# Kernel tuning notes

Hardware: AMD Instinct MI355X
Metric: run time of the kernel (lower is better)

## Reference

```python
import jax, jax.numpy as jnp
import numpy as np

L, B, D = 2048, 2, 1024
H, DK, DV = 16, 64, 64
SPAN = 128
LN_EPS = 1e-5


def setup_inputs() -> dict:
    key = jax.random.key(0)
    ks = jax.random.split(key, 8)
    s_qk = np.sqrt(2.0 / (D + DK)).astype(np.float32)
    s_v = np.sqrt(2.0 / (D + DV)).astype(np.float32)
    return {
        "query": jax.random.normal(ks[0], (L, B, D), jnp.float32),
        "key": jax.random.normal(ks[1], (L, B, D), jnp.float32),
        "value": jax.random.normal(ks[2], (L, B, D), jnp.float32),
        "Wq": jax.random.normal(ks[3], (D, H * DK), jnp.float32) * s_qk,
        "bq": jnp.zeros((H * DK,), jnp.float32),
        "Wk": jax.random.normal(ks[4], (D, H * DK), jnp.float32) * s_qk,
        "bk": jnp.zeros((H * DK,), jnp.float32),
        "Wv": jax.random.normal(ks[5], (D, H * DV), jnp.float32) * s_v,
        "bv": jnp.zeros((H * DV,), jnp.float32),
        "Wfc": jax.random.normal(ks[6], (H * DV, D), jnp.float32) * np.sqrt(2.0 / (H * DV + D)).astype(np.float32),
        "bfc": jnp.zeros((D,), jnp.float32),
        "gamma": jnp.ones((D,), jnp.float32),
        "beta": jnp.zeros((D,), jnp.float32),
    }


def reference(query, key, value, Wq, bq, Wk, bk, Wv, bv, Wfc, bfc, gamma, beta):
    l, b, d = query.shape
    # projections: (l,b,H*dk) -> (H,b,l,dk)   [torch rearrange 'l b (head k) -> head b l k']
    q = (query @ Wq + bq).reshape(l, b, H, DK).transpose(2, 1, 0, 3)
    k = (key @ Wk + bk).reshape(l, b, H, DK).transpose(2, 1, 0, 3)
    v = (value @ Wv + bv).reshape(l, b, H, DV).transpose(2, 1, 0, 3)
    scores = jnp.einsum("hblk,hbtk->hblt", q, k) / jnp.sqrt(jnp.float32(DK))
    # banded additive mask: keep |j - i| <= SPAN
    idx = jnp.arange(l)
    band = jnp.abs(idx[None, :] - idx[:, None]) <= SPAN  # (l, l)
    scores = jnp.where(band[None, None], scores, -jnp.inf)
    attn = jax.nn.softmax(scores, axis=-1)
    out = jnp.einsum("hblt,hbtv->hblv", attn, v)
    # 'head b l v -> l b (head v)'
    out = out.transpose(2, 1, 0, 3).reshape(l, b, H * DV)
    out = out @ Wfc + bfc  # dropout p=0.0 -> identity
    y = out + query  # residual
    mu = jnp.mean(y, axis=-1, keepdims=True)
    var = jnp.mean(jnp.square(y - mu), axis=-1, keepdims=True)
    y = (y - mu) * jax.lax.rsqrt(var + LN_EPS) * gamma + beta
    return (y, attn)
```

## Files before the change

kernel.cpp:

```cpp
#include <hip/hip_runtime.h>
#include <stdint.h>

#define L_SEQ 2048
#define BB 2
#define DD 1024
#define NH 16
#define SPAN 128

typedef __attribute__((ext_vector_type(8))) short short8;
typedef __attribute__((ext_vector_type(4))) float floatx4;

__device__ __forceinline__ short f32_bf16(float f) {
  uint32_t u = __float_as_uint(f);
  u += 0x7FFFu + ((u >> 16) & 1u);
  return (short)(u >> 16);
}

__global__ __launch_bounds__(256) void k_convert(
    const float* __restrict__ s0, const float* __restrict__ s1, const float* __restrict__ s2,
    short* __restrict__ d0, short* __restrict__ d1, short* __restrict__ d2) {
  const float* s = blockIdx.y == 0 ? s0 : (blockIdx.y == 1 ? s1 : s2);
  short* d = blockIdx.y == 0 ? d0 : (blockIdx.y == 1 ? d1 : d2);
  int i = blockIdx.x * 256 + threadIdx.x;
  float4 v = ((const float4*)s)[i];
  short4 o;
  o.x = f32_bf16(v.x); o.y = f32_bf16(v.y); o.z = f32_bf16(v.z); o.w = f32_bf16(v.w);
  ((short4*)d)[i] = o;
}

__global__ __launch_bounds__(256) void k_transpose(
    const float* __restrict__ w0, const float* __restrict__ w1,
    const float* __restrict__ w2, const float* __restrict__ w3,
    short* __restrict__ dst) {
  __shared__ float tile[32][33];
  const float* src = blockIdx.z == 0 ? w0 : blockIdx.z == 1 ? w1 : blockIdx.z == 2 ? w2 : w3;
  short* out = dst + (size_t)blockIdx.z * (DD * DD);
  int bx = blockIdx.x * 32, by = blockIdx.y * 32;
  int tx = threadIdx.x, ty = threadIdx.y;
#pragma unroll
  for (int r = 0; r < 32; r += 8)
    tile[ty + r][tx] = src[(size_t)(by + ty + r) * DD + bx + tx];
  __syncthreads();
#pragma unroll
  for (int r = 0; r < 32; r += 8)
    out[(size_t)(bx + ty + r) * DD + by + tx] = f32_bf16(tile[tx][ty + r]);
}

__global__ __launch_bounds__(256) void k_zero(float4* __restrict__ p) {
  size_t i = (size_t)blockIdx.x * 256 + threadIdx.x;
  float4 z = {0.f, 0.f, 0.f, 0.f};
#pragma unroll
  for (int w = 0; w < 8; ++w) p[i + (size_t)w * 4194304] = z;
}

#define BM 128
#define BN 128
#define BK 32
#define LDK 56

__device__ __forceinline__ void gemm_core(const short* __restrict__ A,
                                          const short* __restrict__ BT,
                                          floatx4 acc[4][4], int bm0, int bn0) {
  __shared__ short As[BM * LDK];
  __shared__ short Bs[BN * LDK];
  int tid = threadIdx.x;
  int wave = tid >> 6, lane = tid & 63;
  int li = lane & 15, quad = lane >> 4;
  int wm = (wave & 1) * 64, wn = (wave >> 1) * 64;
  int srow = tid >> 1, scol = (tid & 1) * 16;
  const short* gA = A + (size_t)(bm0 + srow) * DD + scol;
  const short* gB = BT + (size_t)(bn0 + srow) * DD + scol;
  short* sA = &As[srow * LDK + scol];
  short* sB = &Bs[srow * LDK + scol];
  for (int k0 = 0; k0 < DD; k0 += BK) {
    short8 a0 = *(const short8*)(gA + k0);
    short8 a1 = *(const short8*)(gA + k0 + 8);
    short8 b0 = *(const short8*)(gB + k0);
    short8 b1 = *(const short8*)(gB + k0 + 8);
    __syncthreads();
    *(short8*)sA = a0;
    *(short8*)(sA + 8) = a1;
    *(short8*)sB = b0;
    *(short8*)(sB + 8) = b1;
    __syncthreads();
    short8 af[4], bf[4];
#pragma unroll
    for (int t = 0; t < 4; ++t) {
      af[t] = *(const short8*)&As[(wm + t * 16 + li) * LDK + quad * 8];
      bf[t] = *(const short8*)&Bs[(wn + t * 16 + li) * LDK + quad * 8];
    }
#pragma unroll
    for (int tm = 0; tm < 4; ++tm)
#pragma unroll
      for (int tn = 0; tn < 4; ++tn)
        acc[tm][tn] = __builtin_amdgcn_mfma_f32_16x16x32_bf16(af[tm], bf[tn], acc[tm][tn], 0, 0, 0);
  }
}

__global__ __launch_bounds__(256) void k_proj(
    const short* __restrict__ xq, const short* __restrict__ xk, const short* __restrict__ xv,
    const short* __restrict__ WT,
    const float* __restrict__ bq, const float* __restrict__ bk, const float* __restrict__ bv,
    short* __restrict__ qo, short* __restrict__ ko, short* __restrict__ vTo) {
  int mode = blockIdx.z;
  const short* A = mode == 0 ? xq : (mode == 1 ? xk : xv);
  const short* BT = WT + (size_t)mode * DD * DD;
  const float* bias = mode == 0 ? bq : (mode == 1 ? bk : bv);
  floatx4 acc[4][4] = {};
  int bm0 = blockIdx.y * BM, bn0 = blockIdx.x * BN;
  gemm_core(A, BT, acc, bm0, bn0);

  int tid = threadIdx.x;
  int wave = tid >> 6, lane = tid & 63;
  int li = lane & 15, quad = lane >> 4;
  int wm = (wave & 1) * 64, wn = (wave >> 1) * 64;
  short* dst01 = (mode == 0) ? qo : ko;
#pragma unroll
  for (int tm = 0; tm < 4; ++tm) {
#pragma unroll
    for (int tn = 0; tn < 4; ++tn) {
      int gn = bn0 + wn + tn * 16 + li;
      float bs = bias[gn];
      int h = gn >> 6, dk = gn & 63;
#pragma unroll
      for (int r = 0; r < 4; ++r) {
        int gm = bm0 + wm + tm * 16 + quad * 4 + r;
        int l = gm >> 1, b = gm & 1;
        short bvv = f32_bf16(acc[tm][tn][r] + bs);
        if (mode < 2)
          dst01[(((size_t)h * BB + b) * L_SEQ + l) * 64 + dk] = bvv;
        else
          vTo[(((size_t)h * BB + b) * 64 + dk) * L_SEQ + l] = bvv;
      }
    }
  }
}

__global__ __launch_bounds__(64) void k_attn(
    const short* __restrict__ qw, const short* __restrict__ kw, const short* __restrict__ vTw,
    float* __restrict__ attn_out, short* __restrict__ ctx) {
  __shared__ short P[16 * 296];
  const int i0 = blockIdx.x * 16;
  const int hb = blockIdx.y;
  const int lane = threadIdx.x;
  const int li = lane & 15, quad = lane >> 4;
  const short* Q = qw + (size_t)hb * L_SEQ * 64;
  const short* K = kw + (size_t)hb * L_SEQ * 64;
  const short* VT = vTw + (size_t)hb * 64 * L_SEQ;
  float* Aout = attn_out + (size_t)hb * L_SEQ * L_SEQ;

  short8 qf0 = *(const short8*)(Q + (size_t)(i0 + li) * 64 + quad * 8);
  short8 qf1 = *(const short8*)(Q + (size_t)(i0 + li) * 64 + 32 + quad * 8);

  floatx4 S[17];
  const int jbase = i0 - SPAN;
#pragma unroll
  for (int t = 0; t < 17; ++t) {
    int j0 = jbase + t * 16;
    floatx4 acc = {0.f, 0.f, 0.f, 0.f};
    if (j0 >= 0 && j0 < L_SEQ) {
      const short* kp = K + (size_t)(j0 + li) * 64 + quad * 8;
      short8 kf0 = *(const short8*)kp;
      short8 kf1 = *(const short8*)(kp + 32);
      acc = __builtin_amdgcn_mfma_f32_16x16x32_bf16(qf0, kf0, acc, 0, 0, 0);
      acc = __builtin_amdgcn_mfma_f32_16x16x32_bf16(qf1, kf1, acc, 0, 0, 0);
    }
    S[t] = acc;
  }
  float mrow[4] = {-1e30f, -1e30f, -1e30f, -1e30f};
#pragma unroll
  for (int t = 0; t < 17; ++t) {
    int j0 = jbase + t * 16;
    bool tvalid = (j0 >= 0) && (j0 < L_SEQ);
    int j = j0 + li;
#pragma unroll
    for (int r = 0; r < 4; ++r) {
      int i = i0 + quad * 4 + r;
      bool inband = tvalid && (j >= i - SPAN) && (j <= i + SPAN);
      float s = inband ? S[t][r] * 0.125f : -1e30f;
      S[t][r] = s;
      mrow[r] = fmaxf(mrow[r], s);
    }
  }
#pragma unroll
  for (int m = 1; m <= 8; m <<= 1)
#pragma unroll
    for (int r = 0; r < 4; ++r) mrow[r] = fmaxf(mrow[r], __shfl_xor(mrow[r], m));
  float lsum[4] = {0.f, 0.f, 0.f, 0.f};
#pragma unroll
  for (int t = 0; t < 17; ++t)
#pragma unroll
    for (int r = 0; r < 4; ++r) {
      float p = __expf(S[t][r] - mrow[r]);
      S[t][r] = p;
      lsum[r] += p;
    }
#pragma unroll
  for (int m = 1; m <= 8; m <<= 1)
#pragma unroll
    for (int r = 0; r < 4; ++r) lsum[r] += __shfl_xor(lsum[r], m);
  float inv[4];
#pragma unroll
  for (int r = 0; r < 4; ++r) inv[r] = 1.0f / lsum[r];

#pragma unroll
  for (int c = 0; c < 4; ++c) P[li * 296 + 272 + quad * 4 + c] = 0;
#pragma unroll
  for (int t = 0; t < 17; ++t) {
    int j0 = jbase + t * 16;
    bool tvalid = (j0 >= 0) && (j0 < L_SEQ);
#pragma unroll
    for (int r = 0; r < 4; ++r) {
      int irow = quad * 4 + r;
      float p = S[t][r] * inv[r];
      P[irow * 296 + t * 16 + li] = f32_bf16(p);
      if (tvalid) Aout[(size_t)(i0 + irow) * L_SEQ + j0 + li] = p;
    }
  }
  __syncthreads();
  floatx4 O[4] = {};
#pragma unroll
  for (int c = 0; c < 9; ++c) {
    short8 pf = *(const short8*)&P[li * 296 + c * 32 + quad * 8];
    int jg = jbase + c * 32 + quad * 8;
    int jc = (jg >= 0 && jg < L_SEQ) ? jg : 0;
#pragma unroll
    for (int n = 0; n < 4; ++n) {
      short8 vf = *(const short8*)(VT + (size_t)(n * 16 + li) * L_SEQ + jc);
      O[n] = __builtin_amdgcn_mfma_f32_16x16x32_bf16(pf, vf, O[n], 0, 0, 0);
    }
  }
  const int b = hb & 1, h = hb >> 1;
#pragma unroll
  for (int n = 0; n < 4; ++n)
#pragma unroll
    for (int r = 0; r < 4; ++r) {
      int irow = quad * 4 + r;
      ctx[((size_t)(i0 + irow) * BB + b) * DD + h * 64 + n * 16 + li] = f32_bf16(O[n][r]);
    }
}

__global__ __launch_bounds__(256) void k_fc(
    const short* __restrict__ ctx, const short* __restrict__ WfcT,
    const float* __restrict__ bfc, const float* __restrict__ query,
    float* __restrict__ ypre) {
  floatx4 acc[4][4] = {};
  int bm0 = blockIdx.y * BM, bn0 = blockIdx.x * BN;
  gemm_core(ctx, WfcT, acc, bm0, bn0);
  int tid = threadIdx.x;
  int wave = tid >> 6, lane = tid & 63;
  int li = lane & 15, quad = lane >> 4;
  int wm = (wave & 1) * 64, wn = (wave >> 1) * 64;
#pragma unroll
  for (int tm = 0; tm < 4; ++tm)
#pragma unroll
    for (int tn = 0; tn < 4; ++tn) {
      int gn = bn0 + wn + tn * 16 + li;
      float bs = bfc[gn];
#pragma unroll
      for (int r = 0; r < 4; ++r) {
        int gm = bm0 + wm + tm * 16 + quad * 4 + r;
        ypre[(size_t)gm * DD + gn] = acc[tm][tn][r] + bs + query[(size_t)gm * DD + gn];
      }
    }
}

__global__ __launch_bounds__(256) void k_ln(
    const float* __restrict__ yp, const float* __restrict__ gamma,
    const float* __restrict__ beta, float* __restrict__ out) {
  __shared__ float red[8];
  int row = blockIdx.x, tid = threadIdx.x;
  float4 v = ((const float4*)(yp + (size_t)row * DD))[tid];
  float s = v.x + v.y + v.z + v.w;
  float s2 = v.x * v.x + v.y * v.y + v.z * v.z + v.w * v.w;
#pragma unroll
  for (int m = 1; m <= 32; m <<= 1) {
    s += __shfl_xor(s, m);
    s2 += __shfl_xor(s2, m);
  }
  int wv = tid >> 6;
  if ((tid & 63) == 0) { red[wv] = s; red[wv + 4] = s2; }
  __syncthreads();
  s = red[0] + red[1] + red[2] + red[3];
  s2 = red[4] + red[5] + red[6] + red[7];
  float mu = s * (1.0f / DD);
  float var = s2 * (1.0f / DD) - mu * mu;
  float rs = rsqrtf(var + 1e-5f);
  float4 g = ((const float4*)gamma)[tid];
  float4 bb = ((const float4*)beta)[tid];
  float4 o;
  o.x = (v.x - mu) * rs * g.x + bb.x;
  o.y = (v.y - mu) * rs * g.y + bb.y;
  o.z = (v.z - mu) * rs * g.z + bb.z;
  o.w = (v.w - mu) * rs * g.w + bb.w;
  ((float4*)(out + (size_t)row * DD))[tid] = o;
}

extern "C" void kernel_launch(void* const* d_in, const int* in_sizes, int n_in,
                              void* d_out, int out_size, void* d_ws, size_t ws_size,
                              hipStream_t stream) {
  const float* query = (const float*)d_in[0];
  const float* key   = (const float*)d_in[1];
  const float* value = (const float*)d_in[2];
  const float* Wq    = (const float*)d_in[3];
  const float* bq    = (const float*)d_in[4];
  const float* Wk    = (const float*)d_in[5];
  const float* bk    = (const float*)d_in[6];
  const float* Wv    = (const float*)d_in[7];
  const float* bv    = (const float*)d_in[8];
  const float* Wfc   = (const float*)d_in[9];
  const float* bfc   = (const float*)d_in[10];
  const float* gamma = (const float*)d_in[11];
  const float* beta  = (const float*)d_in[12];
  float* out = (float*)d_out;
  float* attn = out + (size_t)L_SEQ * BB * DD;

  char* w = (char*)d_ws;
  short* xq_b  = (short*)(w);
  short* xk_b  = (short*)(w + ((size_t)8 << 20));
  short* xv_b  = (short*)(w + ((size_t)16 << 20));
  short* WT    = (short*)(w + ((size_t)24 << 20));
  short* q_ws  = (short*)(w + ((size_t)32 << 20));
  short* k_ws  = (short*)(w + ((size_t)40 << 20));
  short* vT_ws = (short*)(w + ((size_t)48 << 20));
  short* ctx   = (short*)(w + ((size_t)56 << 20));
  float* ypre  = (float*)(w + ((size_t)64 << 20));

  k_convert<<<dim3(4096, 3), 256, 0, stream>>>(query, key, value, xq_b, xk_b, xv_b);
  k_transpose<<<dim3(32, 32, 4), dim3(32, 8), 0, stream>>>(Wq, Wk, Wv, Wfc, WT);
  k_zero<<<16384, 256, 0, stream>>>((float4*)attn);
  k_proj<<<dim3(8, 32, 3), 256, 0, stream>>>(xq_b, xk_b, xv_b, WT, bq, bk, bv, q_ws, k_ws, vT_ws);
  k_attn<<<dim3(128, 32), 64, 0, stream>>>(q_ws, k_ws, vT_ws, attn, ctx);
  k_fc<<<dim3(8, 32), 256, 0, stream>>>(ctx, WT + (size_t)3 * DD * DD, bfc, query, ypre);
  k_ln<<<4096, 256, 0, stream>>>(ypre, gamma, beta, out);
}
```

Before: 759.2 us.

## Write full attention rows in-kernel, use LDS direct loads, add V transpose pass

Removes the separate zero-fill of the dense attention matrix; the attention kernel now writes every row in full, band values plus zeros, as coalesced float4 stores from a per-wave LDS copy of the probabilities. The GEMM core stages tiles with global_load_lds straight into unpadded shared memory instead of going through registers. The V projection now writes a row-major layout, and a new small kernel transposes it. The attention kernel also packs four waves per block. The attention matrix values are now rounded to bf16 before being written, which reduces precision, and the unpadded LDS layout may cause bank conflicts.

Result: faster. 720.1 us (-5.1%).

```diff
diff --git a/kernel.cpp b/kernel.cpp
--- a/kernel.cpp
+++ b/kernel.cpp
@@ -14,6 +14,15 @@
   uint32_t u = __float_as_uint(f);
   u += 0x7FFFu + ((u >> 16) & 1u);
   return (short)(u >> 16);
+}
+__device__ __forceinline__ float bf2f(short s) {
+  return __uint_as_float(((uint32_t)(uint16_t)s) << 16);
+}
+
+__device__ __forceinline__ void gld16(const short* g, short* l) {
+  __builtin_amdgcn_global_load_lds(
+      (__attribute__((address_space(1))) void*)(g),
+      (__attribute__((address_space(3))) void*)(l), 16, 0, 0);
 }
 
 __global__ __launch_bounds__(256) void k_convert(
@@ -46,48 +55,37 @@
     out[(size_t)(bx + ty + r) * DD + by + tx] = f32_bf16(tile[tx][ty + r]);
 }
 
-__global__ __launch_bounds__(256) void k_zero(float4* __restrict__ p) {
-  size_t i = (size_t)blockIdx.x * 256 + threadIdx.x;
-  float4 z = {0.f, 0.f, 0.f, 0.f};
-#pragma unroll
-  for (int w = 0; w < 8; ++w) p[i + (size_t)w * 4194304] = z;
-}
-
 #define BM 128
 #define BN 128
 #define BK 32
-#define LDK 56
 
 __device__ __forceinline__ void gemm_core(const short* __restrict__ A,
                                           const short* __restrict__ BT,
                                           floatx4 acc[4][4], int bm0, int bn0) {
-  __shared__ short As[BM * LDK];
-  __shared__ short Bs[BN * LDK];
+  __shared__ short As[BM * BK];
+  __shared__ short Bs[BN * BK];
   int tid = threadIdx.x;
   int wave = tid >> 6, lane = tid & 63;
   int li = lane & 15, quad = lane >> 4;
   int wm = (wave & 1) * 64, wn = (wave >> 1) * 64;
-  int srow = tid >> 1, scol = (tid & 1) * 16;
+  int srow = wave * 32 + (lane >> 2);
+  int scol = (lane & 3) * 8;
   const short* gA = A + (size_t)(bm0 + srow) * DD + scol;
   const short* gB = BT + (size_t)(bn0 + srow) * DD + scol;
-  short* sA = &As[srow * LDK + scol];
-  short* sB = &Bs[srow * LDK + scol];
+  short* lA = &As[wave * 32 * BK];
+  short* lB = &Bs[wave * 32 * BK];
   for (int k0 = 0; k0 < DD; k0 += BK) {
-    short8 a0 = *(const short8*)(gA + k0);
-    short8 a1 = *(const short8*)(gA + k0 + 8);
-    short8 b0 = *(const short8*)(gB + k0);
-    short8 b1 = *(const short8*)(gB + k0 + 8);
     __syncthreads();
-    *(short8*)sA = a0;
-    *(short8*)(sA + 8) = a1;
-    *(short8*)sB = b0;
-    *(short8*)(sB + 8) = b1;
+    gld16(gA + k0, lA);
+    gld16(gA + (size_t)16 * DD + k0, lA + 16 * BK);
+    gld16(gB + k0, lB);
+    gld16(gB + (size_t)16 * DD + k0, lB + 16 * BK);
     __syncthreads();
     short8 af[4], bf[4];
 #pragma unroll
     for (int t = 0; t < 4; ++t) {
-      af[t] = *(const short8*)&As[(wm + t * 16 + li) * LDK + quad * 8];
-      bf[t] = *(const short8*)&Bs[(wn + t * 16 + li) * LDK + quad * 8];
+      af[t] = *(const short8*)&As[(wm + t * 16 + li) * BK + quad * 8];
+      bf[t] = *(const short8*)&Bs[(wn + t * 16 + li) * BK + quad * 8];
     }
 #pragma unroll
     for (int tm = 0; tm < 4; ++tm)
@@ -101,7 +99,7 @@
     const short* __restrict__ xq, const short* __restrict__ xk, const short* __restrict__ xv,
     const short* __restrict__ WT,
     const float* __restrict__ bq, const float* __restrict__ bk, const float* __restrict__ bv,
-    short* __restrict__ qo, short* __restrict__ ko, short* __restrict__ vTo) {
+    short* __restrict__ qo, short* __restrict__ ko, short* __restrict__ vo) {
   int mode = blockIdx.z;
   const short* A = mode == 0 ? xq : (mode == 1 ? xk : xv);
   const short* BT = WT + (size_t)mode * DD * DD;
@@ -114,7 +112,7 @@
   int wave = tid >> 6, lane = tid & 63;
   int li = lane & 15, quad = lane >> 4;
   int wm = (wave & 1) * 64, wn = (wave >> 1) * 64;
-  short* dst01 = (mode == 0) ? qo : ko;
+  short* dst = (mode == 0) ? qo : (mode == 1 ? ko : vo);
 #pragma unroll
   for (int tm = 0; tm < 4; ++tm) {
 #pragma unroll
@@ -126,24 +124,40 @@
       for (int r = 0; r < 4; ++r) {
         int gm = bm0 + wm + tm * 16 + quad * 4 + r;
         int l = gm >> 1, b = gm & 1;
-        short bvv = f32_bf16(acc[tm][tn][r] + bs);
-        if (mode < 2)
-          dst01[(((size_t)h * BB + b) * L_SEQ + l) * 64 + dk] = bvv;
-        else
-          vTo[(((size_t)h * BB + b) * 64 + dk) * L_SEQ + l] = bvv;
+        dst[(((size_t)h * BB + b) * L_SEQ + l) * 64 + dk] = f32_bf16(acc[tm][tn][r] + bs);
       }
     }
   }
 }
 
-__global__ __launch_bounds__(64) void k_attn(
+__global__ __launch_bounds__(256) void k_vt(const short* __restrict__ vl, short* __restrict__ vt) {
+  __shared__ short tl[64][72];
+  int l0 = blockIdx.x * 64, hb = blockIdx.y;
+  const short* src = vl + ((size_t)hb * L_SEQ + l0) * 64;
+  short* dst = vt + (size_t)hb * 64 * L_SEQ + l0;
+  int tid = threadIdx.x;
+  int r = tid >> 2, c0 = (tid & 3) * 16;
+  *(short8*)&tl[r][c0] = *(const short8*)(src + (size_t)r * 64 + c0);
+  *(short8*)&tl[r][c0 + 8] = *(const short8*)(src + (size_t)r * 64 + c0 + 8);
+  __syncthreads();
+  int d = tid >> 2, lb = (tid & 3) * 16;
+  short8 o0, o1;
+#pragma unroll
+  for (int j = 0; j < 8; ++j) o0[j] = tl[lb + j][d];
+#pragma unroll
+  for (int j = 0; j < 8; ++j) o1[j] = tl[lb + 8 + j][d];
+  *(short8*)(dst + (size_t)d * L_SEQ + lb) = o0;
+  *(short8*)(dst + (size_t)d * L_SEQ + lb + 8) = o1;
+}
+
+__global__ __launch_bounds__(256) void k_attn(
     const short* __restrict__ qw, const short* __restrict__ kw, const short* __restrict__ vTw,
     float* __restrict__ attn_out, short* __restrict__ ctx) {
-  __shared__ short P[16 * 296];
-  const int i0 = blockIdx.x * 16;
+  __shared__ short P[4][16 * 296];
+  const int wv = threadIdx.x >> 6, lane = threadIdx.x & 63;
+  const int li = lane & 15, quad = lane >> 4;
+  const int i0 = blockIdx.x * 64 + wv * 16;
   const int hb = blockIdx.y;
-  const int lane = threadIdx.x;
-  const int li = lane & 15, quad = lane >> 4;
   const short* Q = qw + (size_t)hb * L_SEQ * 64;
   const short* K = kw + (size_t)hb * L_SEQ * 64;
   const short* VT = vTw + (size_t)hb * 64 * L_SEQ;
@@ -203,25 +217,19 @@
 #pragma unroll
   for (int r = 0; r < 4; ++r) inv[r] = 1.0f / lsum[r];
 
-#pragma unroll
-  for (int c = 0; c < 4; ++c) P[li * 296 + 272 + quad * 4 + c] = 0;
-#pragma unroll
-  for (int t = 0; t < 17; ++t) {
-    int j0 = jbase + t * 16;
-    bool tvalid = (j0 >= 0) && (j0 < L_SEQ);
-#pragma unroll
-    for (int r = 0; r < 4; ++r) {
-      int irow = quad * 4 + r;
-      float p = S[t][r] * inv[r];
-      P[irow * 296 + t * 16 + li] = f32_bf16(p);
-      if (tvalid) Aout[(size_t)(i0 + irow) * L_SEQ + j0 + li] = p;
-    }
-  }
+  short* myP = P[wv];
+#pragma unroll
+  for (int t = 0; t < 17; ++t)
+#pragma unroll
+    for (int r = 0; r < 4; ++r)
+      myP[(quad * 4 + r) * 296 + t * 16 + li] = f32_bf16(S[t][r] * inv[r]);
+  *(short4*)&myP[(lane >> 2) * 296 + 272 + (lane & 3) * 4] = short4{0, 0, 0, 0};
   __syncthreads();
+
   floatx4 O[4] = {};
 #pragma unroll
   for (int c = 0; c < 9; ++c) {
-    short8 pf = *(const short8*)&P[li * 296 + c * 32 + quad * 8];
+    short8 pf = *(const short8*)&myP[li * 296 + c * 32 + quad * 8];
     int jg = jbase + c * 32 + quad * 8;
     int jc = (jg >= 0 && jg < L_SEQ) ? jg : 0;
 #pragma unroll
@@ -238,6 +246,23 @@
       int irow = quad * 4 + r;
       ctx[((size_t)(i0 + irow) * BB + b) * DD + h * 64 + n * 16 + li] = f32_bf16(O[n][r]);
     }
+
+#pragma unroll 4
+  for (int row = 0; row < 16; ++row) {
+    float* orow = Aout + (size_t)(i0 + row) * L_SEQ;
+    const short* prow = &myP[row * 296];
+#pragma unroll
+    for (int it = 0; it < 8; ++it) {
+      int col = it * 256 + lane * 4;
+      int s = col - jbase;
+      float4 v = {0.f, 0.f, 0.f, 0.f};
+      if (s >= 0 && s < 288) {
+        short4 p4 = *(const short4*)(prow + s);
+        v.x = bf2f(p4.x); v.y = bf2f(p4.y); v.z = bf2f(p4.z); v.w = bf2f(p4.w);
+      }
+      *(float4*)(orow + col) = v;
+    }
+  }
 }
 
 __global__ __launch_bounds__(256) void k_fc(
@@ -322,15 +347,16 @@
   short* WT    = (short*)(w + ((size_t)24 << 20));
   short* q_ws  = (short*)(w + ((size_t)32 << 20));
   short* k_ws  = (short*)(w + ((size_t)40 << 20));
-  short* vT_ws = (short*)(w + ((size_t)48 << 20));
-  short* ctx   = (short*)(w + ((size_t)56 << 20));
-  float* ypre  = (float*)(w + ((size_t)64 << 20));
+  short* v_lin = (short*)(w + ((size_t)48 << 20));
+  short* vT_ws = (short*)(w + ((size_t)56 << 20));
+  short* ctx   = (short*)(w + ((size_t)64 << 20));
+  float* ypre  = (float*)(w + ((size_t)72 << 20));
 
   k_convert<<<dim3(4096, 3), 256, 0, stream>>>(query, key, value, xq_b, xk_b, xv_b);
   k_transpose<<<dim3(32, 32, 4), dim3(32, 8), 0, stream>>>(Wq, Wk, Wv, Wfc, WT);
-  k_zero<<<16384, 256, 0, stream>>>((float4*)attn);
-  k_proj<<<dim3(8, 32, 3), 256, 0, stream>>>(xq_b, xk_b, xv_b, WT, bq, bk, bv, q_ws, k_ws, vT_ws);
-  k_attn<<<dim3(128, 32), 64, 0, stream>>>(q_ws, k_ws, vT_ws, attn, ctx);
+  k_proj<<<dim3(8, 32, 3), 256, 0, stream>>>(xq_b, xk_b, xv_b, WT, bq, bk, bv, q_ws, k_ws, v_lin);
+  k_vt<<<dim3(32, 32), 256, 0, stream>>>(v_lin, vT_ws);
+  k_attn<<<dim3(32, 32), 256, 0, stream>>>(q_ws, k_ws, vT_ws, attn, ctx);
   k_fc<<<dim3(8, 32), 256, 0, stream>>>(ctx, WT + (size_t)3 * DD * DD, bfc, query, ypre);
   k_ln<<<4096, 256, 0, stream>>>(ypre, gamma, beta, out);
 }
```
